# Kernel optimization log

Hardware: AMD Instinct MI355X
Metric: run time of the kernel (lower is better)

Reference implementation:

```python
import jax, jax.numpy as jnp
import numpy as np

B, S, IN_DIM, OUT_DIM, G = 8, 2048, 512, 256, 8
CHUNK = 128  # positions per scan step; per-chunk phi = CHUNK*O*O*G floats
EPS = 1e-5   # torch LayerNorm default


def make_periods():
    # periods[i,j,g] = i*(O*G) + j*G + g + 2
    i = jnp.arange(OUT_DIM, dtype=jnp.float32)[:, None, None]
    j = jnp.arange(OUT_DIM, dtype=jnp.float32)[None, :, None]
    g = jnp.arange(G, dtype=jnp.float32)[None, None, :]
    return i * (OUT_DIM * G) + j * G + g + 2.0


def setup_inputs() -> dict:
    key = jax.random.key(0)
    ks = jax.random.split(key, 4)
    x = jax.random.normal(ks[0], (B, S, IN_DIM), dtype=jnp.float32)
    positions = jnp.arange(S, dtype=jnp.int64 if jax.config.jax_enable_x64 else jnp.int32)
    M = jax.random.uniform(ks[1], (OUT_DIM, IN_DIM), minval=-0.5, maxval=0.5, dtype=jnp.float32)
    P = jax.random.uniform(ks[2], (OUT_DIM, OUT_DIM, G), minval=-0.1, maxval=0.1, dtype=jnp.float32)
    W_res = jax.random.uniform(ks[3], (OUT_DIM, IN_DIM), minval=-0.1, maxval=0.1, dtype=jnp.float32)
    ln_scale = jnp.ones((OUT_DIM,), dtype=jnp.float32)
    ln_bias = jnp.zeros((OUT_DIM,), dtype=jnp.float32)
    periods = make_periods()
    return {"x": x, "M": M, "P": P, "W_res": W_res, "ln_scale": ln_scale,
            "ln_bias": ln_bias, "periods": periods, "positions": positions}


def layer_norm(h, scale, bias):
    mu = jnp.mean(h, axis=-1, keepdims=True)
    var = jnp.mean(jnp.square(h - mu), axis=-1, keepdims=True)  # biased, like torch
    return (h - mu) * jax.lax.rsqrt(var + EPS) * scale + bias


def reference(x, M, P, W_res, ln_scale, ln_bias, periods, positions):
    # x: (B,S,in), M: (out,in), P: (out,out,G), periods: (out,out,G)
    x_trans = layer_norm(jnp.einsum('bsi,oi->bso', x, M), ln_scale, ln_bias)

    two_pi = jnp.float32(2.0 * np.pi)
    pos_chunks = positions.astype(jnp.float32).reshape(-1, CHUNK)  # (S/CHUNK, CHUNK)

    def body(carry, pos):
        # phi: (CHUNK, O, O, G); reduce over g first to avoid the huge 5D tensor
        phi = jnp.cos(two_pi * pos[:, None, None, None] / periods)
        A = jnp.einsum('sijg,ijg->sij', phi, P)  # (CHUNK, O, O)
        return carry, A

    _, A = jax.lax.scan(body, 0, pos_chunks)
    A = A.reshape(S, OUT_DIM, OUT_DIM)  # A[s,i,j] = sum_g P[i,j,g]*cos(2*pi*k_s/T_ijg)

    Nk = jnp.einsum('bsj,sij->bsi', x_trans, A)  # (B,S,out)
    residual = jnp.einsum('bsi,oi->bso', x, W_res)  # separate residual proj
    return Nk + residual
```

## Files before the change

kernel.cpp:

```cpp
#include <hip/hip_runtime.h>
#include <hip/hip_bf16.h>
#include <math.h>

#define B_   8
#define S_   2048
#define IN_  512
#define OUT_ 256
#define G_   8


typedef float  f32x4  __attribute__((ext_vector_type(4)));
typedef short  s16x8  __attribute__((ext_vector_type(8)));
typedef __bf16 bf16x8 __attribute__((ext_vector_type(8)));
typedef unsigned short u16x8 __attribute__((ext_vector_type(8)));

__device__ __forceinline__ float cos2pi(float f) {
#if __has_builtin(__builtin_amdgcn_cosf)
    return __builtin_amdgcn_cosf(f);
#else
    return __cosf(6.28318530717958647692f * f);
#endif
}

__device__ __forceinline__ float fractf_(float f) {
#if __has_builtin(__builtin_amdgcn_fractf)
    return __builtin_amdgcn_fractf(f);
#else
    return f - floorf(f);
#endif
}

__device__ __forceinline__ unsigned short f2bf(float f) {
    unsigned u = __builtin_bit_cast(unsigned, f);
    u += 0x7fffu + ((u >> 16) & 1u);
    return (unsigned short)(u >> 16);
}

template <typename T>
__device__ __forceinline__ auto atomF_(T* p, T v, int) -> decltype(unsafeAtomicAdd(p, v)) {
    return unsafeAtomicAdd(p, v);
}
template <typename T>
__device__ __forceinline__ T atomF_(T* p, T v, long) {
    return atomicAdd(p, v);
}
__device__ __forceinline__ void atomAddF(float* p, float v) { atomF_(p, v, 0); }

template <typename T>
__device__ __forceinline__ auto mfma_bf16_(T a, T b, f32x4 c, int)
    -> decltype(__builtin_amdgcn_mfma_f32_16x16x32_bf16(a, b, c, 0, 0, 0)) {
    return __builtin_amdgcn_mfma_f32_16x16x32_bf16(a, b, c, 0, 0, 0);
}
template <typename T>
__device__ __forceinline__ auto mfma_bf16_(T a, T b, f32x4 c, long)
    -> decltype(__builtin_amdgcn_mfma_f32_16x16x32_bf16(__builtin_bit_cast(bf16x8, a),
                                                        __builtin_bit_cast(bf16x8, b), c, 0, 0, 0)) {
    return __builtin_amdgcn_mfma_f32_16x16x32_bf16(__builtin_bit_cast(bf16x8, a),
                                                   __builtin_bit_cast(bf16x8, b), c, 0, 0, 0);
}
__device__ __forceinline__ f32x4 mfma_bf16(s16x8 a, s16x8 b, f32x4 c) {
    return mfma_bf16_(a, b, c, 0);
}

__device__ __forceinline__ void gld16(const void* g, void* l) {
    __builtin_amdgcn_global_load_lds((const __attribute__((address_space(1))) unsigned int*)g,
                                     (__attribute__((address_space(3))) unsigned int*)l,
                                     16, 0, 0);
}

__global__ __launch_bounds__(256) void cvt_xw(const float* __restrict__ x,
                                              const float* __restrict__ M,
                                              const float* __restrict__ Wres,
                                              unsigned short* __restrict__ Xb,
                                              unsigned short* __restrict__ Wb) {
    const int bid = blockIdx.x;
    const float* src;
    unsigned short* dst;
    if (bid < 4096) {
        const int idx = bid * 256 + threadIdx.x;
        src = x + (size_t)idx * 8;
        dst = Xb + (size_t)idx * 8;
    } else {
        const int idx = (bid - 4096) * 256 + threadIdx.x;
        const int row = idx >> 6;
        const int col = (idx & 63) * 8;
        src = (row < 256) ? (M + (size_t)row * 512 + col)
                          : (Wres + (size_t)(row - 256) * 512 + col);
        dst = Wb + (size_t)row * 512 + col;
    }
    const float4 v0 = *(const float4*)(src);
    const float4 v1 = *(const float4*)(src + 4);
    u16x8 o;
    o[0] = f2bf(v0.x); o[1] = f2bf(v0.y); o[2] = f2bf(v0.z); o[3] = f2bf(v0.w);
    o[4] = f2bf(v1.x); o[5] = f2bf(v1.y); o[6] = f2bf(v1.z); o[7] = f2bf(v1.w);
    *(u16x8*)dst = o;
}

__global__ __launch_bounds__(256) void gemm_mfma(const unsigned short* __restrict__ Xb,
                                                 const unsigned short* __restrict__ Wb,
                                                 float* __restrict__ y,
                                                 float* __restrict__ out) {
    __shared__ __align__(16) unsigned short At[64 * 64];
    __shared__ __align__(16) unsigned short Bt[128 * 64];
    const int t    = threadIdx.x;
    const int col0 = blockIdx.x * 128;
    const int row0 = blockIdx.y * 64;

    const unsigned short* ga[2]; int la[2];
    const unsigned short* gb[4]; int lb[4];
#pragma unroll
    for (int cc = 0; cc < 2; ++cc) {
        const int L = cc * 256 + t;
        const int r = L >> 3;
        const int c = (L & 7) ^ (r & 7);
        ga[cc] = Xb + (size_t)(row0 + r) * 512 + c * 8;
        la[cc] = L * 8;
    }
#pragma unroll
    for (int cc = 0; cc < 4; ++cc) {
        const int L = cc * 256 + t;
        const int r = L >> 3;
        const int c = (L & 7) ^ (r & 7);
        gb[cc] = Wb + (size_t)(col0 + r) * 512 + c * 8;
        lb[cc] = L * 8;
    }

    const int lane = t & 63;
    const int wave = t >> 6;
    const int wn   = wave * 32;
    const int quad = lane >> 4;
    const int l16  = lane & 15;

    f32x4 acc[4][2];
#pragma unroll
    for (int mi = 0; mi < 4; ++mi)
#pragma unroll
        for (int ni = 0; ni < 2; ++ni) acc[mi][ni] = {0.0f, 0.0f, 0.0f, 0.0f};

    for (int k0 = 0; k0 < 512; k0 += 64) {
        __syncthreads();
#pragma unroll
        for (int cc = 0; cc < 2; ++cc) gld16(ga[cc] + k0, At + la[cc]);
#pragma unroll
        for (int cc = 0; cc < 4; ++cc) gld16(gb[cc] + k0, Bt + lb[cc]);
        __syncthreads();
#pragma unroll
        for (int ks = 0; ks < 2; ++ks) {
            const int cc = (ks * 4 + quad) ^ (l16 & 7);
            s16x8 af[4], bf[2];
#pragma unroll
            for (int mi = 0; mi < 4; ++mi) {
                const int ra = mi * 16 + l16;
                af[mi] = *(const s16x8*)(At + (ra * 8 + cc) * 8);
            }
#pragma unroll
            for (int ni = 0; ni < 2; ++ni) {
                const int rb = wn + ni * 16 + l16;
                bf[ni] = *(const s16x8*)(Bt + (rb * 8 + cc) * 8);
            }
#pragma unroll
            for (int mi = 0; mi < 4; ++mi)
#pragma unroll
                for (int ni = 0; ni < 2; ++ni)
                    acc[mi][ni] = mfma_bf16(af[mi], bf[ni], acc[mi][ni]);
        }
    }

    float* dst   = (col0 < 256) ? y : out;
    const int cb = (col0 & 255) + wn;
#pragma unroll
    for (int mi = 0; mi < 4; ++mi) {
        const int rbase = row0 + mi * 16 + quad * 4;
#pragma unroll
        for (int ni = 0; ni < 2; ++ni) {
            const int col = cb + ni * 16 + l16;
#pragma unroll
            for (int rg = 0; rg < 4; ++rg)
                dst[(size_t)(rbase + rg) * 256 + col] = acc[mi][ni][rg];
        }
    }
}

__global__ __launch_bounds__(256) void gemm_kernel(const float* __restrict__ x,
                                                   const float* __restrict__ M,
                                                   const float* __restrict__ Wres,
                                                   float* __restrict__ y,
                                                   float* __restrict__ out) {
    __shared__ float As[8][132];
    __shared__ float Bs[8][132];
    const int ct = blockIdx.x;
    const int rt = blockIdx.y;
    const int t  = threadIdx.x;
    const int row0 = rt * 128;
    const float* W = (ct < 2) ? M : Wres;
    const int wcol0 = (ct & 1) * 128;
    float acc[8][8];
#pragma unroll
    for (int r = 0; r < 8; ++r)
#pragma unroll
        for (int c = 0; c < 8; ++c) acc[r][c] = 0.0f;
    const int lr = t >> 1;
    const int lk = (t & 1) << 2;
    for (int k0 = 0; k0 < 512; k0 += 8) {
        float4 av = *(const float4*)(x + (size_t)(row0 + lr) * 512 + k0 + lk);
        float4 bv = *(const float4*)(W + (size_t)(wcol0 + lr) * 512 + k0 + lk);
        __syncthreads();
        As[lk + 0][lr] = av.x; As[lk + 1][lr] = av.y; As[lk + 2][lr] = av.z; As[lk + 3][lr] = av.w;
        Bs[lk + 0][lr] = bv.x; Bs[lk + 1][lr] = bv.y; Bs[lk + 2][lr] = bv.z; Bs[lk + 3][lr] = bv.w;
        __syncthreads();
        const int tx = t & 15, ty = t >> 4;
#pragma unroll
        for (int kk = 0; kk < 8; ++kk) {
            const float4 a0 = *(const float4*)&As[kk][ty * 8];
            const float4 a1 = *(const float4*)&As[kk][ty * 8 + 4];
            const float4 b0 = *(const float4*)&Bs[kk][tx * 8];
            const float4 b1 = *(const float4*)&Bs[kk][tx * 8 + 4];
            const float ar[8] = {a0.x, a0.y, a0.z, a0.w, a1.x, a1.y, a1.z, a1.w};
            const float br[8] = {b0.x, b0.y, b0.z, b0.w, b1.x, b1.y, b1.z, b1.w};
#pragma unroll
            for (int r = 0; r < 8; ++r)
#pragma unroll
                for (int c = 0; c < 8; ++c) acc[r][c] = fmaf(ar[r], br[c], acc[r][c]);
        }
    }
    const int tx = t & 15, ty = t >> 4;
    float* dst = (ct < 2) ? y : out;
    const int cbase = (ct & 1) * 128 + tx * 8;
#pragma unroll
    for (int r = 0; r < 8; ++r) {
        float4 v0 = {acc[r][0], acc[r][1], acc[r][2], acc[r][3]};
        float4 v1 = {acc[r][4], acc[r][5], acc[r][6], acc[r][7]};
        float* p = dst + (size_t)(row0 + ty * 8 + r) * 256 + cbase;
        *(float4*)(p)     = v0;
        *(float4*)(p + 4) = v1;
    }
}

__global__ __launch_bounds__(256) void ln_kernel(float* __restrict__ y,
                                                 const float* __restrict__ scale,
                                                 const float* __restrict__ bias) {
    const int t    = threadIdx.x;
    const int row  = blockIdx.x * 4 + (t >> 6);
    const int lane = t & 63;
    float* p = y + (size_t)row * 256 + lane * 4;
    float4 v = *(float4*)p;
    float s  = v.x + v.y + v.z + v.w;
    float ss = v.x * v.x + v.y * v.y + v.z * v.z + v.w * v.w;
#pragma unroll
    for (int off = 32; off > 0; off >>= 1) {
        s  += __shfl_xor(s, off);
        ss += __shfl_xor(ss, off);
    }
    const float mu  = s * (1.0f / 256.0f);
    const float var = ss * (1.0f / 256.0f) - mu * mu;
    const float rs  = rsqrtf(var + 1e-5f);
    float4 sc = *(const float4*)(scale + lane * 4);
    float4 bi = *(const float4*)(bias + lane * 4);
    float4 o;
    o.x = (v.x - mu) * rs * sc.x + bi.x;
    o.y = (v.y - mu) * rs * sc.y + bi.y;
    o.z = (v.z - mu) * rs * sc.z + bi.z;
    o.w = (v.w - mu) * rs * sc.w + bi.w;
    *(float4*)p = o;
}

__global__ __launch_bounds__(256) void prep_ptk(const float* __restrict__ P,
                                                const float* __restrict__ periods,
                                                float4* __restrict__ PTK) {
    const int tid = blockIdx.x * 256 + threadIdx.x;
    const int j = tid >> 8, i = tid & 255;
    float p[8], iT[8], k2[8];
#pragma unroll
    for (int g = 0; g < 8; ++g) {
        const int idx = (i * 256 + j) * 8 + g;
        p[g]  = P[idx];
        iT[g] = 1.0f / periods[idx];
        k2[g] = 2.0f * cos2pi(iT[g]);
    }
    float4* base = PTK + (size_t)(j * 6) * 256 + i;
    base[0]    = make_float4(p[0], iT[0], p[1], iT[1]);
    base[256]  = make_float4(p[2], iT[2], p[3], iT[3]);
    base[512]  = make_float4(p[4], iT[4], p[5], iT[5]);
    base[768]  = make_float4(p[6], iT[6], p[7], iT[7]);
    base[1024] = make_float4(k2[0], k2[1], k2[2], k2[3]);
    base[1280] = make_float4(k2[4], k2[5], k2[6], k2[7]);
}

__global__ __launch_bounds__(256, 4) void cosnk_js(const float4* __restrict__ PTK,
                                                   const float* __restrict__ xt,
                                                   float* __restrict__ out) {
    __shared__ float xs[128 * 64];
    const int t  = threadIdx.x;
    const int bx = blockIdx.x;
    const int ih = (bx >> 2) & 1;
    const int rid = ((bx >> 3) << 2) | (bx & 3);
    const int stile = rid >> 1;
    const int jh = rid & 1;
    const int s0 = stile * 8;
    const int jbase = jh * 128;

    {
        const int slot = t >> 2;
        const int st   = slot >> 3;
        const int b    = slot & 7;
        const int jg   = t & 3;
        const float* src = xt + (size_t)(b * S_ + s0 + st) * 256 + jbase + jg * 32;
#pragma unroll
        for (int q = 0; q < 8; ++q) {
            float4 v = *(const float4*)(src + 4 * q);
            const int jl = jg * 32 + 4 * q;
            xs[(jl + 0) * 64 + slot] = v.x;
            xs[(jl + 1) * 64 + slot] = v.y;
            xs[(jl + 2) * 64 + slot] = v.z;
            xs[(jl + 3) * 64 + slot] = v.w;
        }
    }
    __syncthreads();

    const int i   = ih * 128 + (t & 127);
    const int jq  = t >> 7;
    const int jl0 = jq * 64;
    const float sv0 = (float)s0;

    float acc[8][8];
#pragma unroll
    for (int s = 0; s < 8; ++s)
#pragma unroll
        for (int b = 0; b < 8; ++b) acc[s][b] = 0.0f;

    const float4* ptk = PTK + (size_t)(jbase + jl0) * 1536 + i;
    float4 q0 = ptk[0],    q1 = ptk[256],  q2 = ptk[512];
    float4 q3 = ptk[768], k01 = ptk[1024], k23 = ptk[1280];

#define CHEB8(p_, iT_, k2_)                         \
    do {                                            \
        float f0 = fractf_(sv0 * (iT_));            \
        float c0 = cos2pi(f0);                      \
        float c1 = cos2pi(fractf_(f0 + (iT_)));     \
        float c2 = fmaf((k2_), c1, -c0);            \
        float c3 = fmaf((k2_), c2, -c1);            \
        float c4 = fmaf((k2_), c3, -c2);            \
        float c5 = fmaf((k2_), c4, -c3);            \
        float c6 = fmaf((k2_), c5, -c4);            \
        float c7 = fmaf((k2_), c6, -c5);            \
        a0 = fmaf((p_), c0, a0); a1 = fmaf((p_), c1, a1); \
        a2 = fmaf((p_), c2, a2); a3 = fmaf((p_), c3, a3); \
        a4 = fmaf((p_), c4, a4); a5 = fmaf((p_), c5, a5); \
        a6 = fmaf((p_), c6, a6); a7 = fmaf((p_), c7, a7); \
    } while (0)

    for (int jj = 0; jj < 64; ++jj) {
        const float4* pn = ptk + ((jj < 63) ? 1536 : 0);
        const float4 n0 = pn[0],   n1 = pn[256],  n2 = pn[512];
        const float4 n3 = pn[768], n4 = pn[1024], n5 = pn[1280];

        float a0 = 0.f, a1 = 0.f, a2 = 0.f, a3 = 0.f, a4 = 0.f, a5 = 0.f, a6 = 0.f, a7 = 0.f;
        CHEB8(q0.x, q0.y, k01.x);
        CHEB8(q0.z, q0.w, k01.y);
        CHEB8(q1.x, q1.y, k01.z);
        CHEB8(q1.z, q1.w, k01.w);
        CHEB8(q2.x, q2.y, k23.x);
        CHEB8(q2.z, q2.w, k23.y);
        CHEB8(q3.x, q3.y, k23.z);
        CHEB8(q3.z, q3.w, k23.w);

        const float* xrow = &xs[(jl0 + jj) * 64];
        const float as_[8] = {a0, a1, a2, a3, a4, a5, a6, a7};
#pragma unroll
        for (int s = 0; s < 8; ++s) {
            const float4 xa = *(const float4*)(xrow + s * 8);
            const float4 xb = *(const float4*)(xrow + s * 8 + 4);
            acc[s][0] = fmaf(as_[s], xa.x, acc[s][0]);
            acc[s][1] = fmaf(as_[s], xa.y, acc[s][1]);
            acc[s][2] = fmaf(as_[s], xa.z, acc[s][2]);
            acc[s][3] = fmaf(as_[s], xa.w, acc[s][3]);
            acc[s][4] = fmaf(as_[s], xb.x, acc[s][4]);
            acc[s][5] = fmaf(as_[s], xb.y, acc[s][5]);
            acc[s][6] = fmaf(as_[s], xb.z, acc[s][6]);
            acc[s][7] = fmaf(as_[s], xb.w, acc[s][7]);
        }
        q0 = n0; q1 = n1; q2 = n2; q3 = n3; k01 = n4; k23 = n5;
        ptk = pn;
    }
#undef CHEB8

    __syncthreads();
    const int tl = t & 127;
    if (jq) {
#pragma unroll
        for (int slot = 0; slot < 64; ++slot)
            xs[slot * 128 + tl] = acc[slot >> 3][slot & 7];
    }
    __syncthreads();
    if (!jq) {
#pragma unroll
        for (int slot = 0; slot < 64; ++slot) {
            const int st = slot >> 3, b = slot & 7;
            const float v = acc[st][b] + xs[slot * 128 + tl];
            atomAddF(&out[(size_t)(b * S_ + s0 + st) * 256 + i], v);
        }
    }
}

extern "C" void kernel_launch(void* const* d_in, const int* in_sizes, int n_in,
                              void* d_out, int out_size, void* d_ws, size_t ws_size,
                              hipStream_t stream) {
    const float* x        = (const float*)d_in[0];
    const float* M        = (const float*)d_in[1];
    const float* P        = (const float*)d_in[2];
    const float* Wres     = (const float*)d_in[3];
    const float* ln_scale = (const float*)d_in[4];
    const float* ln_bias  = (const float*)d_in[5];
    const float* periods  = (const float*)d_in[6];

    float* out = (float*)d_out;
    char*  wsb = (char*)d_ws;
    float* y   = (float*)wsb;
    unsigned short* Xb = (unsigned short*)(wsb + (size_t)16 * 1024 * 1024);
    float4* PTK        = (float4*)(wsb + (size_t)16 * 1024 * 1024);
    unsigned short* Wb = (unsigned short*)(wsb + (size_t)32 * 1024 * 1024);

    const bool use_mfma = (ws_size >= (size_t)34078720);

    if (use_mfma) {
        cvt_xw<<<4224, 256, 0, stream>>>(x, M, Wres, Xb, Wb);
        dim3 ggrid(4, 256);
        gemm_mfma<<<ggrid, 256, 0, stream>>>(Xb, Wb, y, out);
    } else {
        dim3 ggrid(4, 128);
        gemm_kernel<<<ggrid, 256, 0, stream>>>(x, M, Wres, y, out);
    }

    ln_kernel<<<4096, 256, 0, stream>>>(y, ln_scale, ln_bias);

    prep_ptk<<<256, 256, 0, stream>>>(P, periods, PTK);

    cosnk_js<<<1024, 256, 0, stream>>>(PTK, y, out);
}
```

Before: 236.1 us.

## Fuse LayerNorm into cos kernel and merge PTK prep into convert kernel

Removes the standalone LayerNorm pass. The cos/accumulate kernel now reads the pre-norm rows, computes the row mean and variance with shuffles, and normalizes while staging into shared memory. The PTK precompute is folded into the bf16 convert launch as extra blocks when the workspace is large enough, which means relocating PTK so it no longer aliases Xb. Together this saves two launches and a full read/write of y. In exchange, each block now reads entire 256-wide rows to compute statistics, doubling its global reads of y, and the new path depends on the workspace size.

```diff
diff --git a/kernel.cpp b/kernel.cpp
--- a/kernel.cpp
+++ b/kernel.cpp
@@ -66,6 +66,62 @@
     __builtin_amdgcn_global_load_lds((const __attribute__((address_space(1))) unsigned int*)g,
                                      (__attribute__((address_space(3))) unsigned int*)l,
                                      16, 0, 0);
+}
+
+__device__ __forceinline__ void prep_one(const float* __restrict__ P,
+                                         const float* __restrict__ periods,
+                                         float4* __restrict__ PTK, int tid) {
+    const int j = tid >> 8, i = tid & 255;
+    float p[8], iT[8], k2[8];
+#pragma unroll
+    for (int g = 0; g < 8; ++g) {
+        const int idx = (i * 256 + j) * 8 + g;
+        p[g]  = P[idx];
+        iT[g] = 1.0f / periods[idx];
+        k2[g] = 2.0f * cos2pi(iT[g]);
+    }
+    float4* base = PTK + (size_t)(j * 6) * 256 + i;
+    base[0]    = make_float4(p[0], iT[0], p[1], iT[1]);
+    base[256]  = make_float4(p[2], iT[2], p[3], iT[3]);
+    base[512]  = make_float4(p[4], iT[4], p[5], iT[5]);
+    base[768]  = make_float4(p[6], iT[6], p[7], iT[7]);
+    base[1024] = make_float4(k2[0], k2[1], k2[2], k2[3]);
+    base[1280] = make_float4(k2[4], k2[5], k2[6], k2[7]);
+}
+
+__global__ __launch_bounds__(256) void cvt_prep(const float* __restrict__ x,
+                                                const float* __restrict__ M,
+                                                const float* __restrict__ Wres,
+                                                const float* __restrict__ P,
+                                                const float* __restrict__ periods,
+                                                unsigned short* __restrict__ Xb,
+                                                unsigned short* __restrict__ Wb,
+                                                float4* __restrict__ PTK) {
+    const int bid = blockIdx.x;
+    if (bid >= 4224) {
+        prep_one(P, periods, PTK, (bid - 4224) * 256 + threadIdx.x);
+        return;
+    }
+    const float* src;
+    unsigned short* dst;
+    if (bid < 4096) {
+        const int idx = bid * 256 + threadIdx.x;
+        src = x + (size_t)idx * 8;
+        dst = Xb + (size_t)idx * 8;
+    } else {
+        const int idx = (bid - 4096) * 256 + threadIdx.x;
+        const int row = idx >> 6;
+        const int col = (idx & 63) * 8;
+        src = (row < 256) ? (M + (size_t)row * 512 + col)
+                          : (Wres + (size_t)(row - 256) * 512 + col);
+        dst = Wb + (size_t)row * 512 + col;
+    }
+    const float4 v0 = *(const float4*)(src);
+    const float4 v1 = *(const float4*)(src + 4);
+    u16x8 o;
+    o[0] = f2bf(v0.x); o[1] = f2bf(v0.y); o[2] = f2bf(v0.z); o[3] = f2bf(v0.w);
+    o[4] = f2bf(v1.x); o[5] = f2bf(v1.y); o[6] = f2bf(v1.z); o[7] = f2bf(v1.w);
+    *(u16x8*)dst = o;
 }
 
 __global__ __launch_bounds__(256) void cvt_xw(const float* __restrict__ x,
@@ -96,6 +152,12 @@
     *(u16x8*)dst = o;
 }
 
+__global__ __launch_bounds__(256) void prep_ptk(const float* __restrict__ P,
+                                                const float* __restrict__ periods,
+                                                float4* __restrict__ PTK) {
+    prep_one(P, periods, PTK, blockIdx.x * 256 + threadIdx.x);
+}
+
 __global__ __launch_bounds__(256) void gemm_mfma(const unsigned short* __restrict__ Xb,
                                                  const unsigned short* __restrict__ Wb,
                                                  float* __restrict__ y,
@@ -236,59 +298,11 @@
     }
 }
 
-__global__ __launch_bounds__(256) void ln_kernel(float* __restrict__ y,
-                                                 const float* __restrict__ scale,
-                                                 const float* __restrict__ bias) {
-    const int t    = threadIdx.x;
-    const int row  = blockIdx.x * 4 + (t >> 6);
-    const int lane = t & 63;
-    float* p = y + (size_t)row * 256 + lane * 4;
-    float4 v = *(float4*)p;
-    float s  = v.x + v.y + v.z + v.w;
-    float ss = v.x * v.x + v.y * v.y + v.z * v.z + v.w * v.w;
-#pragma unroll
-    for (int off = 32; off > 0; off >>= 1) {
-        s  += __shfl_xor(s, off);
-        ss += __shfl_xor(ss, off);
-    }
-    const float mu  = s * (1.0f / 256.0f);
-    const float var = ss * (1.0f / 256.0f) - mu * mu;
-    const float rs  = rsqrtf(var + 1e-5f);
-    float4 sc = *(const float4*)(scale + lane * 4);
-    float4 bi = *(const float4*)(bias + lane * 4);
-    float4 o;
-    o.x = (v.x - mu) * rs * sc.x + bi.x;
-    o.y = (v.y - mu) * rs * sc.y + bi.y;
-    o.z = (v.z - mu) * rs * sc.z + bi.z;
-    o.w = (v.w - mu) * rs * sc.w + bi.w;
-    *(float4*)p = o;
-}
-
-__global__ __launch_bounds__(256) void prep_ptk(const float* __restrict__ P,
-                                                const float* __restrict__ periods,
-                                                float4* __restrict__ PTK) {
-    const int tid = blockIdx.x * 256 + threadIdx.x;
-    const int j = tid >> 8, i = tid & 255;
-    float p[8], iT[8], k2[8];
-#pragma unroll
-    for (int g = 0; g < 8; ++g) {
-        const int idx = (i * 256 + j) * 8 + g;
-        p[g]  = P[idx];
-        iT[g] = 1.0f / periods[idx];
-        k2[g] = 2.0f * cos2pi(iT[g]);
-    }
-    float4* base = PTK + (size_t)(j * 6) * 256 + i;
-    base[0]    = make_float4(p[0], iT[0], p[1], iT[1]);
-    base[256]  = make_float4(p[2], iT[2], p[3], iT[3]);
-    base[512]  = make_float4(p[4], iT[4], p[5], iT[5]);
-    base[768]  = make_float4(p[6], iT[6], p[7], iT[7]);
-    base[1024] = make_float4(k2[0], k2[1], k2[2], k2[3]);
-    base[1280] = make_float4(k2[4], k2[5], k2[6], k2[7]);
-}
-
-__global__ __launch_bounds__(256, 4) void cosnk_js(const float4* __restrict__ PTK,
-                                                   const float* __restrict__ xt,
-                                                   float* __restrict__ out) {
+__global__ __launch_bounds__(256, 4) void cosnk_lnjs(const float4* __restrict__ PTK,
+                                                     const float* __restrict__ ypre,
+                                                     const float* __restrict__ ln_scale,
+                                                     const float* __restrict__ ln_bias,
+                                                     float* __restrict__ out) {
     __shared__ float xs[128 * 64];
     const int t  = threadIdx.x;
     const int bx = blockIdx.x;
@@ -304,15 +318,32 @@
         const int st   = slot >> 3;
         const int b    = slot & 7;
         const int jg   = t & 3;
-        const float* src = xt + (size_t)(b * S_ + s0 + st) * 256 + jbase + jg * 32;
-#pragma unroll
-        for (int q = 0; q < 8; ++q) {
-            float4 v = *(const float4*)(src + 4 * q);
-            const int jl = jg * 32 + 4 * q;
-            xs[(jl + 0) * 64 + slot] = v.x;
-            xs[(jl + 1) * 64 + slot] = v.y;
-            xs[(jl + 2) * 64 + slot] = v.z;
-            xs[(jl + 3) * 64 + slot] = v.w;
+        const float* src = ypre + (size_t)(b * S_ + s0 + st) * 256 + jg * 64;
+        float4 v[16];
+        float sum = 0.0f, ssq = 0.0f;
+#pragma unroll
+        for (int q = 0; q < 16; ++q) {
+            v[q] = *(const float4*)(src + 4 * q);
+            sum += v[q].x + v[q].y + v[q].z + v[q].w;
+            ssq += v[q].x * v[q].x + v[q].y * v[q].y + v[q].z * v[q].z + v[q].w * v[q].w;
+        }
+        sum += __shfl_xor(sum, 1); sum += __shfl_xor(sum, 2);
+        ssq += __shfl_xor(ssq, 1); ssq += __shfl_xor(ssq, 2);
+        const float mu  = sum * (1.0f / 256.0f);
+        const float var = ssq * (1.0f / 256.0f) - mu * mu;
+        const float rs  = rsqrtf(var + 1e-5f);
+        if ((jg >> 1) == jh) {
+            const int jl0s = (jg & 1) * 64;
+#pragma unroll
+            for (int q = 0; q < 16; ++q) {
+                const float4 sc = *(const float4*)(ln_scale + jg * 64 + 4 * q);
+                const float4 bi = *(const float4*)(ln_bias  + jg * 64 + 4 * q);
+                const int jl = jl0s + 4 * q;
+                xs[(jl + 0) * 64 + slot] = (v[q].x - mu) * rs * sc.x + bi.x;
+                xs[(jl + 1) * 64 + slot] = (v[q].y - mu) * rs * sc.y + bi.y;
+                xs[(jl + 2) * 64 + slot] = (v[q].z - mu) * rs * sc.z + bi.z;
+                xs[(jl + 3) * 64 + slot] = (v[q].w - mu) * rs * sc.w + bi.w;
+            }
         }
     }
     __syncthreads();
@@ -415,25 +446,32 @@
 
     float* out = (float*)d_out;
     char*  wsb = (char*)d_ws;
-    float* y   = (float*)wsb;
-    unsigned short* Xb = (unsigned short*)(wsb + (size_t)16 * 1024 * 1024);
-    float4* PTK        = (float4*)(wsb + (size_t)16 * 1024 * 1024);
-    unsigned short* Wb = (unsigned short*)(wsb + (size_t)32 * 1024 * 1024);
-
-    const bool use_mfma = (ws_size >= (size_t)34078720);
-
-    if (use_mfma) {
+    const size_t MB = 1024 * 1024;
+    float* y = (float*)wsb;
+    unsigned short* Xb = (unsigned short*)(wsb + 16 * MB);
+    unsigned short* Wb = (unsigned short*)(wsb + 32 * MB);
+
+    const bool big  = (ws_size >= 39 * MB);
+    const bool mfma = (ws_size >= (size_t)34078720);
+
+    float4* PTK;
+    if (big) {
+        PTK = (float4*)(wsb + 33 * MB);
+        cvt_prep<<<4480, 256, 0, stream>>>(x, M, Wres, P, periods, Xb, Wb, PTK);
+        dim3 ggrid(4, 256);
+        gemm_mfma<<<ggrid, 256, 0, stream>>>(Xb, Wb, y, out);
+    } else if (mfma) {
+        PTK = (float4*)(wsb + 16 * MB);
         cvt_xw<<<4224, 256, 0, stream>>>(x, M, Wres, Xb, Wb);
         dim3 ggrid(4, 256);
         gemm_mfma<<<ggrid, 256, 0, stream>>>(Xb, Wb, y, out);
+        prep_ptk<<<256, 256, 0, stream>>>(P, periods, PTK);
     } else {
+        PTK = (float4*)(wsb + 16 * MB);
         dim3 ggrid(4, 128);
         gemm_kernel<<<ggrid, 256, 0, stream>>>(x, M, Wres, y, out);
-    }
-
-    ln_kernel<<<4096, 256, 0, stream>>>(y, ln_scale, ln_bias);
-
-    prep_ptk<<<256, 256, 0, stream>>>(P, periods, PTK);
-
-    cosnk_js<<<1024, 256, 0, stream>>>(PTK, y, out);
-}
+        prep_ptk<<<256, 256, 0, stream>>>(P, periods, PTK);
+    }
+
+    cosnk_lnjs<<<1024, 256, 0, stream>>>(PTK, y, ln_scale, ln_bias, out);
+}
```

Result: slower. 244.5 us (+3.6%).
